# Performance work log

Hardware: AMD Instinct MI355X
Metric: run time of the kernel (lower is better)

The kernel has to match this reference:

```python
import jax, jax.numpy as jnp
import numpy as np

EMBED = 1024
HEADS = 16
HEAD_DIM = EMBED // HEADS
OUT_DIM = 1024


def setup_inputs() -> dict:
    key = jax.random.key(0)
    ks = jax.random.split(key, 8)
    N, L = 2, 2048
    values = jax.random.normal(ks[0], (N, L, EMBED), dtype=jnp.float32)
    keys_t = jax.random.normal(ks[1], (N, L, EMBED), dtype=jnp.float32)
    query = jax.random.normal(ks[2], (N, L, EMBED), dtype=jnp.float32)
    s = 1.0 / np.sqrt(HEAD_DIM)
    Wv = jax.random.normal(ks[3], (HEAD_DIM, HEAD_DIM), dtype=jnp.float32) * s
    Wk = jax.random.normal(ks[4], (HEAD_DIM, HEAD_DIM), dtype=jnp.float32) * s
    Wq = jax.random.normal(ks[5], (HEAD_DIM, HEAD_DIM), dtype=jnp.float32) * s
    Wout = jax.random.normal(ks[6], (OUT_DIM, EMBED), dtype=jnp.float32) * (1.0 / np.sqrt(EMBED))
    bout = jax.random.normal(ks[7], (OUT_DIM,), dtype=jnp.float32) * 0.01
    return {"values": values, "keys": keys_t, "query": query,
            "Wv": Wv, "Wk": Wk, "Wq": Wq, "Wout": Wout, "bout": bout}


def reference(values, keys, query, Wv, Wk, Wq, Wout, bout):
    N, Lq, _ = query.shape
    Lk = keys.shape[1]
    # split into heads: (N, L, H, D)
    v = values.reshape(N, Lk, HEADS, HEAD_DIM)
    k = keys.reshape(N, Lk, HEADS, HEAD_DIM)
    q = query.reshape(N, Lq, HEADS, HEAD_DIM)
    # per-head shared linear projections (torch Linear: x @ W.T, no bias)
    v = jnp.einsum('nlhd,ed->nlhe', v, Wv)
    k = jnp.einsum('nlhd,ed->nlhe', k, Wk)
    q = jnp.einsum('nqhd,ed->nqhe', q, Wq)
    # scores (N, H, Q, K); NOTE: scale is 1/sqrt(embed_size), per original code
    scores = jnp.einsum('nqhd,nkhd->nhqk', q, k) / jnp.sqrt(jnp.float32(EMBED))
    attn = jax.nn.softmax(scores, axis=-1)
    out = jnp.einsum('nhqk,nkhd->nqhd', attn, v).reshape(N, Lq, EMBED)
    # fc_out: x @ Wout.T + bout
    return out @ Wout.T + bout
```

## Files before the change

### kernel.cpp

```cpp
#include <hip/hip_runtime.h>
#include <cstdint>

typedef __attribute__((ext_vector_type(8))) short short8;
typedef __attribute__((ext_vector_type(4))) float floatx4;
typedef __attribute__((ext_vector_type(16))) float floatx16;
typedef __attribute__((ext_vector_type(4))) _Float16 half4;
typedef __attribute__((ext_vector_type(8))) _Float16 half8;

#define DEV __device__ __forceinline__

constexpr int NB = 2, Lseq = 2048, NH = 16, HD = 64, EMB = 1024;
constexpr float QSCALE = 0.03125f * 1.4426950408889634f;

DEV uint32_t pack2(float lo, float hi) {
  uint32_t a = __builtin_bit_cast(uint32_t, lo) + 0x8000u;
  uint32_t b = __builtin_bit_cast(uint32_t, hi) + 0x8000u;
  return __builtin_amdgcn_perm(b, a, 0x07060302);
}

DEV uint32_t packh2(float lo, float hi) {
  return __builtin_bit_cast(uint32_t, __builtin_amdgcn_cvt_pkrtz(lo, hi));
}

DEV void gl_lds16(const void* g, void* l) {
  __builtin_amdgcn_global_load_lds((const __attribute__((address_space(1))) void*)g,
                                   (__attribute__((address_space(3))) void*)l, 16, 0, 0);
}

DEV void pl32(uint32_t& x, uint32_t& y) {
  typedef __attribute__((ext_vector_type(2))) unsigned int uint2v;
  uint2v r = __builtin_amdgcn_permlane32_swap(x, y, false, false);
  x = r[0];
  y = r[1];
}

DEV short8 ld8bf(const float* p, float sc) {
  float4 u = *(const float4*)p;
  float4 v = *(const float4*)(p + 4);
  union { short8 s; uint32_t d[4]; } r;
  r.d[0] = pack2(u.x * sc, u.y * sc);
  r.d[1] = pack2(u.z * sc, u.w * sc);
  r.d[2] = pack2(v.x * sc, v.y * sc);
  r.d[3] = pack2(v.z * sc, v.w * sc);
  return r.s;
}

__global__ __launch_bounds__(256) void prep_kernel(
    const float* __restrict__ values, const float* __restrict__ keysrc,
    const float* __restrict__ query, const float* __restrict__ Wv,
    const float* __restrict__ Wk, const float* __restrict__ Wq,
    const float* __restrict__ Wout,
    uint16_t* __restrict__ qp, uint16_t* __restrict__ kp,
    uint16_t* __restrict__ vp, uint16_t* __restrict__ wbf) {
  const int t = threadIdx.x, w = t >> 6, lane = t & 63;
  const int quad = lane >> 4, l16 = lane & 15;
  const int wid = blockIdx.x * 4 + w;
  const int mat = wid >> 10, sub = wid & 1023;

  if (mat == 3) {
#pragma unroll
    for (int i = 0; i < 4; ++i) {
      int idx = sub * 256 + i * 64 + lane;
      float4 v = ((const float4*)Wout)[idx];
      uint2 p;
      p.x = pack2(v.x, v.y);
      p.y = pack2(v.z, v.w);
      ((uint2*)wbf)[idx] = p;
    }
    return;
  }

  floatx4 c[4][4];
#pragma unroll
  for (int i = 0; i < 4; ++i)
#pragma unroll
    for (int j = 0; j < 4; ++j) c[i][j] = floatx4{0.f, 0.f, 0.f, 0.f};

  if (mat < 2) {
    const float* src = mat ? keysrc : query;
    const float* W   = mat ? Wk : Wq;
    const float asc  = mat ? 1.f : QSCALE;
    uint16_t* dst    = mat ? kp : qp;
    const int R0 = sub * 64;
    short8 a[4][2], b[4][2];
#pragma unroll
    for (int dc = 0; dc < 2; ++dc) {
#pragma unroll
      for (int f = 0; f < 4; ++f) {
        a[f][dc] = ld8bf(W + (size_t)(f * 16 + l16) * 64 + dc * 32 + quad * 8, asc);
        b[f][dc] = ld8bf(src + (size_t)(R0 + f * 16 + l16) * 64 + dc * 32 + quad * 8, 1.f);
      }
    }
#pragma unroll
    for (int dc = 0; dc < 2; ++dc)
#pragma unroll
      for (int mf = 0; mf < 4; ++mf)
#pragma unroll
        for (int nf = 0; nf < 4; ++nf)
          c[mf][nf] = __builtin_amdgcn_mfma_f32_16x16x32_bf16(a[mf][dc], b[nf][dc], c[mf][nf], 0, 0, 0);
#pragma unroll
    for (int nf = 0; nf < 4; ++nf) {
      int r = R0 + nf * 16 + l16;
      int h = r & 15, l = (r >> 4) & 2047, n = r >> 15;
      uint16_t* drow = dst + ((size_t)(n * 16 + h) * 2048 + l) * 64;
#pragma unroll
      for (int mf = 0; mf < 4; ++mf) {
        uint2 pk;
        pk.x = pack2(c[mf][nf][0], c[mf][nf][1]);
        pk.y = pack2(c[mf][nf][2], c[mf][nf][3]);
        *(uint2*)(drow + mf * 16 + quad * 4) = pk;
      }
    }
  } else {
    const int nh = sub >> 5, L0 = (sub & 31) * 64;
    const int n = nh >> 4, h = nh & 15;
    short8 a[4][2], b[4][2];
#pragma unroll
    for (int dc = 0; dc < 2; ++dc) {
#pragma unroll
      for (int f = 0; f < 4; ++f) {
        a[f][dc] = ld8bf(values + (size_t)(n * 2048 + L0 + f * 16 + l16) * 1024 + h * 64 + dc * 32 + quad * 8, 1.f);
        b[f][dc] = ld8bf(Wv + (size_t)(f * 16 + l16) * 64 + dc * 32 + quad * 8, 1.f);
      }
    }
#pragma unroll
    for (int dc = 0; dc < 2; ++dc)
#pragma unroll
      for (int mf = 0; mf < 4; ++mf)
#pragma unroll
        for (int nf = 0; nf < 4; ++nf)
          c[mf][nf] = __builtin_amdgcn_mfma_f32_16x16x32_bf16(a[mf][dc], b[nf][dc], c[mf][nf], 0, 0, 0);
#pragma unroll
    for (int nf = 0; nf < 4; ++nf) {
      int d = nf * 16 + l16;
      uint16_t* drow = vp + ((size_t)nh * 64 + d) * 2048 + L0;
#pragma unroll
      for (int mf = 0; mf < 4; ++mf) {
        uint2 pk;
        pk.x = packh2(c[mf][nf][0], c[mf][nf][1]);
        pk.y = packh2(c[mf][nf][2], c[mf][nf][3]);
        *(uint2*)(drow + mf * 16 + quad * 4) = pk;
      }
    }
  }
}

__global__ __launch_bounds__(128, 2) void flash_kernel(const uint16_t* __restrict__ qp,
                                                       const uint16_t* __restrict__ kp,
                                                       const uint16_t* __restrict__ vp,
                                                       uint16_t* __restrict__ xg) {
  constexpr int kbn = 32;
  __shared__ uint16_t Kt[2][64 * 64];
  __shared__ uint16_t Vt[2][64 * 64];
  const int t = threadIdx.x;
  const int w = t >> 6, lane = t & 63, hi = lane >> 5, l32 = lane & 31;
  const int nh = blockIdx.x, qt = blockIdx.y;
  const int q0w = qt * 64 + w * 32;
  const uint16_t* Qb = qp + (size_t)nh * Lseq * HD;
  const uint16_t* Kb = kp + (size_t)nh * Lseq * HD;
  const uint16_t* Vb = vp + (size_t)nh * HD * Lseq;
  const int srow = lane >> 3, sc8 = (lane & 7) ^ (lane >> 3);

  short8 bq[4];
#pragma unroll
  for (int dc = 0; dc < 4; ++dc)
    bq[dc] = *(const short8*)(Qb + (size_t)(q0w + l32) * 64 + dc * 16 + hi * 8);

  floatx16 o[2], lfr;
#pragma unroll
  for (int r = 0; r < 16; ++r) { o[0][r] = 0.f; o[1][r] = 0.f; lfr[r] = 0.f; }
  const _Float16 one = (_Float16)1.0f;
  const half8 vones = {one, one, one, one, one, one, one, one};

  auto stage = [&](int tile, int buf) {
#pragma unroll
    for (int i = 0; i < 4; ++i) {
      int r0 = w * 32 + i * 8;
      int sc = sc8 ^ i;
      gl_lds16(Kb + (size_t)tile * 4096 + (r0 + srow) * 64 + sc * 8, &Kt[buf][r0 * 64]);
      gl_lds16(Vb + (size_t)(r0 + srow) * Lseq + tile * 64 + sc * 8, &Vt[buf][r0 * 64]);
    }
  };

  stage(0, 0);

  for (int kb = 0; kb < kbn; ++kb) {
    __syncthreads();
    const int cur = kb & 1;
    if (kb + 1 < kbn) stage(kb + 1, cur ^ 1);

#pragma unroll
    for (int kt = 0; kt < 2; ++kt) {
      floatx16 s;
#pragma unroll
      for (int r = 0; r < 16; ++r) s[r] = 0.f;
      const int krow = kt * 32 + l32;
      const int ksw = (krow & 7) ^ ((krow >> 3) & 3);
#pragma unroll
      for (int dc = 0; dc < 4; ++dc) {
        short8 ak = *(const short8*)(&Kt[cur][krow * 64 + (((dc << 1) | hi) ^ ksw) * 8]);
        s = __builtin_amdgcn_mfma_f32_32x32x16_bf16(ak, bq[dc], s, 0, 0, 0);
      }
      uint32_t a0 = packh2(__builtin_amdgcn_exp2f(s[0]), __builtin_amdgcn_exp2f(s[1]));
      uint32_t a1 = packh2(__builtin_amdgcn_exp2f(s[2]), __builtin_amdgcn_exp2f(s[3]));
      uint32_t b0 = packh2(__builtin_amdgcn_exp2f(s[4]), __builtin_amdgcn_exp2f(s[5]));
      uint32_t b1 = packh2(__builtin_amdgcn_exp2f(s[6]), __builtin_amdgcn_exp2f(s[7]));
      uint32_t c0 = packh2(__builtin_amdgcn_exp2f(s[8]), __builtin_amdgcn_exp2f(s[9]));
      uint32_t c1 = packh2(__builtin_amdgcn_exp2f(s[10]), __builtin_amdgcn_exp2f(s[11]));
      uint32_t d0 = packh2(__builtin_amdgcn_exp2f(s[12]), __builtin_amdgcn_exp2f(s[13]));
      uint32_t d1 = packh2(__builtin_amdgcn_exp2f(s[14]), __builtin_amdgcn_exp2f(s[15]));
      pl32(a0, b0); pl32(a1, b1); pl32(c0, d0); pl32(c1, d1);
      union { half8 h; uint32_t u[4]; } f0, f1;
      f0.u[0] = a0; f0.u[1] = a1; f0.u[2] = b0; f0.u[3] = b1;
      f1.u[0] = c0; f1.u[1] = c1; f1.u[2] = d0; f1.u[3] = d1;

      lfr = __builtin_amdgcn_mfma_f32_32x32x16_f16(vones, f0.h, lfr, 0, 0, 0);
      lfr = __builtin_amdgcn_mfma_f32_32x32x16_f16(vones, f1.h, lfr, 0, 0, 0);

#pragma unroll
      for (int dt = 0; dt < 2; ++dt) {
        const int vrow = dt * 32 + l32;
        const int vsw = (vrow & 7) ^ ((vrow >> 3) & 3);
        half8 av0 = *(const half8*)(&Vt[cur][vrow * 64 + ((kt * 4 + hi) ^ vsw) * 8]);
        o[dt] = __builtin_amdgcn_mfma_f32_32x32x16_f16(av0, f0.h, o[dt], 0, 0, 0);
        half8 av1 = *(const half8*)(&Vt[cur][vrow * 64 + ((kt * 4 + 2 + hi) ^ vsw) * 8]);
        o[dt] = __builtin_amdgcn_mfma_f32_32x32x16_f16(av1, f1.h, o[dt], 0, 0, 0);
      }
    }
  }

  const int nn = nh >> 4, h = nh & 15;
  const float inv = __builtin_amdgcn_rcpf(lfr[0]);
  uint16_t* xr = xg + ((size_t)(nn * 2048 + q0w + l32)) * 1024 + h * 64;
#pragma unroll
  for (int dt = 0; dt < 2; ++dt)
#pragma unroll
    for (int rg = 0; rg < 4; ++rg) {
      int dd = dt * 32 + rg * 8 + 4 * hi;
      uint2 pk;
      pk.x = pack2(o[dt][rg * 4] * inv, o[dt][rg * 4 + 1] * inv);
      pk.y = pack2(o[dt][rg * 4 + 2] * inv, o[dt][rg * 4 + 3] * inv);
      *(uint2*)(xr + dd) = pk;
    }
}

__global__ __launch_bounds__(256, 2) void out_gemm(const uint16_t* __restrict__ Xg,
                                                   const uint16_t* __restrict__ Wb,
                                                   const float* __restrict__ bias,
                                                   float* __restrict__ out) {
  __shared__ uint16_t Xt[3][64 * 64];
  __shared__ uint16_t Wt[3][128 * 64];
  const int t = threadIdx.x, w = t >> 6, lane = t & 63, quad = lane >> 4, l16 = lane & 15;
  const int m0 = blockIdx.x * 64, o0 = blockIdx.y * 128;
  const int srow = lane >> 3, sc8 = (lane & 7) ^ (lane >> 3);

  floatx4 acc[8];
#pragma unroll
  for (int j = 0; j < 8; ++j) acc[j] = floatx4{0.f, 0.f, 0.f, 0.f};

  auto stage = [&](int buf, int kt) {
#pragma unroll
    for (int i = 0; i < 2; ++i) {
      int r0 = w * 16 + i * 8;
      gl_lds16(Xg + (size_t)(m0 + r0 + srow) * 1024 + kt * 64 + sc8 * 8, &Xt[buf][r0 * 64]);
    }
#pragma unroll
    for (int i = 0; i < 4; ++i) {
      int r0 = w * 32 + i * 8;
      gl_lds16(Wb + (size_t)(o0 + r0 + srow) * 1024 + kt * 64 + sc8 * 8, &Wt[buf][r0 * 64]);
    }
  };

  stage(0, 0);
  stage(1, 1);

  int cur = 0;
  for (int kt = 0; kt < 16; ++kt) {
    if (kt + 1 < 16) asm volatile("s_waitcnt vmcnt(6)" ::: "memory");
    else             asm volatile("s_waitcnt vmcnt(0)" ::: "memory");
    __builtin_amdgcn_s_barrier();
    if (kt + 2 < 16) {
      int tgt = cur + 2; if (tgt >= 3) tgt -= 3;
      stage(tgt, kt + 2);
    }
#pragma unroll
    for (int kc = 0; kc < 2; ++kc) {
      int ra = w * 16 + l16;
      short8 a = *(const short8*)(&Xt[cur][ra * 64 + ((kc * 4 + quad) ^ (ra & 7)) * 8]);
#pragma unroll
      for (int nf = 0; nf < 8; ++nf) {
        int rb = nf * 16 + l16;
        short8 b = *(const short8*)(&Wt[cur][rb * 64 + ((kc * 4 + quad) ^ (rb & 7)) * 8]);
        acc[nf] = __builtin_amdgcn_mfma_f32_16x16x32_bf16(a, b, acc[nf], 0, 0, 0);
      }
    }
    asm volatile("s_waitcnt lgkmcnt(0)" ::: "memory");
    cur = (cur + 1 == 3) ? 0 : cur + 1;
  }

#pragma unroll
  for (int nf = 0; nf < 8; ++nf) {
    float bv = bias[o0 + nf * 16 + l16];
#pragma unroll
    for (int r = 0; r < 4; ++r)
      out[(size_t)(m0 + w * 16 + quad * 4 + r) * 1024 + o0 + nf * 16 + l16] = acc[nf][r] + bv;
  }
}

extern "C" void kernel_launch(void* const* d_in, const int* in_sizes, int n_in,
                              void* d_out, int out_size, void* d_ws, size_t ws_size,
                              hipStream_t stream) {
  const float* values = (const float*)d_in[0];
  const float* keys   = (const float*)d_in[1];
  const float* query  = (const float*)d_in[2];
  const float* Wv     = (const float*)d_in[3];
  const float* Wk     = (const float*)d_in[4];
  const float* Wq     = (const float*)d_in[5];
  const float* Wout   = (const float*)d_in[6];
  const float* bout   = (const float*)d_in[7];
  float* out = (float*)d_out;
  (void)ws_size;

  uint16_t* ws  = (uint16_t*)d_ws;
  uint16_t* qp  = ws;
  uint16_t* kp  = ws + (size_t)4194304;
  uint16_t* vp  = ws + (size_t)8388608;
  uint16_t* wbf = ws + (size_t)12582912;
  uint16_t* xp  = ws + (size_t)13631488;

  prep_kernel<<<dim3(1024), dim3(256), 0, stream>>>(values, keys, query, Wv, Wk, Wq, Wout,
                                                    qp, kp, vp, wbf);
  flash_kernel<<<dim3(32, 32), dim3(128), 0, stream>>>(qp, kp, vp, xp);
  out_gemm<<<dim3(64, 8), dim3(256), 0, stream>>>(xp, wbf, bout, out);
}
```

Measured before the change: 185.1 us.

## Split attention over key halves and merge partials in output GEMM prologue

The flash kernel now splits the key range into two halves along a third grid dimension and uses 4-wave blocks covering 128 queries. Each half writes unnormalized fp16 partial outputs and row sums to the workspace. The output GEMM loads both partials, adds them, normalizes, and packs to bf16 in LDS before the MFMA loop, so the separate normalized activation buffer is no longer written. This aims for better occupancy and more K/V reuse per block, at the cost of extra partial-output traffic, more work in the GEMM prologue, and fp16 accumulation of unnormalized sums.

```diff
diff --git a/kernel.cpp b/kernel.cpp
--- a/kernel.cpp
+++ b/kernel.cpp
@@ -4,7 +4,6 @@
 typedef __attribute__((ext_vector_type(8))) short short8;
 typedef __attribute__((ext_vector_type(4))) float floatx4;
 typedef __attribute__((ext_vector_type(16))) float floatx16;
-typedef __attribute__((ext_vector_type(4))) _Float16 half4;
 typedef __attribute__((ext_vector_type(8))) _Float16 half8;
 
 #define DEV __device__ __forceinline__
@@ -145,20 +144,22 @@
   }
 }
 
-__global__ __launch_bounds__(128, 2) void flash_kernel(const uint16_t* __restrict__ qp,
+__global__ __launch_bounds__(256, 4) void flash_kernel(const uint16_t* __restrict__ qp,
                                                        const uint16_t* __restrict__ kp,
                                                        const uint16_t* __restrict__ vp,
-                                                       uint16_t* __restrict__ xg) {
-  constexpr int kbn = 32;
+                                                       uint32_t* __restrict__ opart,
+                                                       float* __restrict__ psum) {
+  constexpr int kbn = 16;
   __shared__ uint16_t Kt[2][64 * 64];
   __shared__ uint16_t Vt[2][64 * 64];
   const int t = threadIdx.x;
   const int w = t >> 6, lane = t & 63, hi = lane >> 5, l32 = lane & 31;
-  const int nh = blockIdx.x, qt = blockIdx.y;
-  const int q0w = qt * 64 + w * 32;
+  const int nh = blockIdx.x, qt = blockIdx.y, kh = blockIdx.z;
+  const int q0w = qt * 128 + w * 32;
   const uint16_t* Qb = qp + (size_t)nh * Lseq * HD;
-  const uint16_t* Kb = kp + (size_t)nh * Lseq * HD;
+  const uint16_t* Kb = kp + (size_t)nh * Lseq * HD + (size_t)kh * 1024 * 64;
   const uint16_t* Vb = vp + (size_t)nh * HD * Lseq;
+  const int vcol0 = kh * 1024;
   const int srow = lane >> 3, sc8 = (lane & 7) ^ (lane >> 3);
 
   short8 bq[4];
@@ -174,11 +175,11 @@
 
   auto stage = [&](int tile, int buf) {
 #pragma unroll
-    for (int i = 0; i < 4; ++i) {
-      int r0 = w * 32 + i * 8;
-      int sc = sc8 ^ i;
+    for (int i = 0; i < 2; ++i) {
+      int r0 = w * 16 + i * 8;
+      int sc = sc8 ^ ((w * 2 + i) & 3);
       gl_lds16(Kb + (size_t)tile * 4096 + (r0 + srow) * 64 + sc * 8, &Kt[buf][r0 * 64]);
-      gl_lds16(Vb + (size_t)(r0 + srow) * Lseq + tile * 64 + sc * 8, &Vt[buf][r0 * 64]);
+      gl_lds16(Vb + (size_t)(r0 + srow) * Lseq + vcol0 + tile * 64 + sc * 8, &Vt[buf][r0 * 64]);
     }
   };
 
@@ -229,41 +230,75 @@
     }
   }
 
-  const int nn = nh >> 4, h = nh & 15;
-  const float inv = __builtin_amdgcn_rcpf(lfr[0]);
-  uint16_t* xr = xg + ((size_t)(nn * 2048 + q0w + l32)) * 1024 + h * 64;
+  uint32_t* ob = opart + ((size_t)(((nh * 16 + qt) * 2 + kh) * 4 + w)) * 1024 + lane;
 #pragma unroll
   for (int dt = 0; dt < 2; ++dt)
 #pragma unroll
-    for (int rg = 0; rg < 4; ++rg) {
-      int dd = dt * 32 + rg * 8 + 4 * hi;
-      uint2 pk;
-      pk.x = pack2(o[dt][rg * 4] * inv, o[dt][rg * 4 + 1] * inv);
-      pk.y = pack2(o[dt][rg * 4 + 2] * inv, o[dt][rg * 4 + 3] * inv);
-      *(uint2*)(xr + dd) = pk;
-    }
-}
-
-__global__ __launch_bounds__(256, 2) void out_gemm(const uint16_t* __restrict__ Xg,
+    for (int j = 0; j < 8; ++j)
+      ob[(dt * 8 + j) * 64] = packh2(o[dt][2 * j], o[dt][2 * j + 1]);
+  if (hi == 0)
+    psum[((size_t)((nh * 16 + qt) * 2 + kh)) * 128 + w * 32 + l32] = lfr[0];
+}
+
+__global__ __launch_bounds__(256, 2) void out_gemm(const uint32_t* __restrict__ opart,
+                                                   const float* __restrict__ psum,
                                                    const uint16_t* __restrict__ Wb,
                                                    const float* __restrict__ bias,
                                                    float* __restrict__ out) {
-  __shared__ uint16_t Xt[3][64 * 64];
-  __shared__ uint16_t Wt[3][128 * 64];
+  __shared__ uint16_t Xt[64 * 64];
+  __shared__ uint16_t Wt[2][128 * 64];
   const int t = threadIdx.x, w = t >> 6, lane = t & 63, quad = lane >> 4, l16 = lane & 15;
-  const int m0 = blockIdx.x * 64, o0 = blockIdx.y * 128;
+  const int mblk = blockIdx.x, obk = blockIdx.y;
+  const int nrow = mblk >> 5, qt_src = (mblk & 31) >> 1;
+  const int m0 = mblk * 64, o0 = obk * 128;
+  const int w_src = (mblk & 1) * 2 + (w >> 1);
+  const int kh_l = lane >> 5;
+  const int hi_l = (lane >> 4) & 1;
+  const int l32s = (w & 1) * 16 + (lane & 15);
+  const int src_lane = kh_l * 0 + hi_l * 32 + l32s;
   const int srow = lane >> 3, sc8 = (lane & 7) ^ (lane >> 3);
 
   floatx4 acc[8];
 #pragma unroll
   for (int j = 0; j < 8; ++j) acc[j] = floatx4{0.f, 0.f, 0.f, 0.f};
 
-  auto stage = [&](int buf, int kt) {
-#pragma unroll
-    for (int i = 0; i < 2; ++i) {
-      int r0 = w * 16 + i * 8;
-      gl_lds16(Xg + (size_t)(m0 + r0 + srow) * 1024 + kt * 64 + sc8 * 8, &Xt[buf][r0 * 64]);
-    }
+  uint32_t va[16];
+  float lp;
+
+  auto issue_loads = [&](int h) {
+    int nh2 = nrow * 16 + h;
+    size_t tb = (size_t)((nh2 * 16 + qt_src) * 2 + kh_l);
+    const uint32_t* pa = opart + (tb * 4 + w_src) * 1024 + src_lane;
+#pragma unroll
+    for (int k = 0; k < 16; ++k) va[k] = pa[k * 64];
+    lp = psum[tb * 128 + w_src * 32 + l32s];
+  };
+
+  auto pack_write = [&]() {
+    uint32_t lx = __builtin_bit_cast(uint32_t, lp), ly = lx;
+    pl32(lx, ly);
+    float lpart = __builtin_bit_cast(float, (lane < 32) ? ly : lx);
+    float inv = __builtin_amdgcn_rcpf(lp + lpart);
+    const int ra = w * 16 + (lane & 15);
+    const int rsw = ra & 7;
+#pragma unroll
+    for (int k = 0; k < 16; ++k) {
+      const int dt = k >> 3, j = k & 7;
+      uint32_t own = va[k], x = own, y = own;
+      pl32(x, y);
+      uint32_t part = (lane < 32) ? y : x;
+      union { uint32_t u; _Float16 h[2]; } um, up;
+      um.u = own; up.u = part;
+      float v0 = ((float)um.h[0] + (float)up.h[0]) * inv;
+      float v1 = ((float)um.h[1] + (float)up.h[1]) * inv;
+      const int d0t = (j & 1) * 2 + (j >> 1) * 8;
+      const int d = dt * 32 + d0t + 4 * hi_l;
+      if (lane < 32)
+        *(uint32_t*)(&Xt[ra * 64 + ((d >> 3) ^ rsw) * 8 + (d & 7)]) = pack2(v0, v1);
+    }
+  };
+
+  auto dma_w = [&](int buf, int kt) {
 #pragma unroll
     for (int i = 0; i < 4; ++i) {
       int r0 = w * 32 + i * 8;
@@ -271,22 +306,21 @@
     }
   };
 
-  stage(0, 0);
-  stage(1, 1);
-
-  int cur = 0;
+  issue_loads(0);
+  pack_write();
+  dma_w(0, 0);
+
   for (int kt = 0; kt < 16; ++kt) {
-    if (kt + 1 < 16) asm volatile("s_waitcnt vmcnt(6)" ::: "memory");
-    else             asm volatile("s_waitcnt vmcnt(0)" ::: "memory");
-    __builtin_amdgcn_s_barrier();
-    if (kt + 2 < 16) {
-      int tgt = cur + 2; if (tgt >= 3) tgt -= 3;
-      stage(tgt, kt + 2);
+    const int cur = kt & 1;
+    __syncthreads();
+    if (kt + 1 < 16) {
+      issue_loads(kt + 1);
+      dma_w(cur ^ 1, kt + 1);
     }
 #pragma unroll
     for (int kc = 0; kc < 2; ++kc) {
       int ra = w * 16 + l16;
-      short8 a = *(const short8*)(&Xt[cur][ra * 64 + ((kc * 4 + quad) ^ (ra & 7)) * 8]);
+      short8 a = *(const short8*)(&Xt[ra * 64 + ((kc * 4 + quad) ^ (ra & 7)) * 8]);
 #pragma unroll
       for (int nf = 0; nf < 8; ++nf) {
         int rb = nf * 16 + l16;
@@ -294,8 +328,7 @@
         acc[nf] = __builtin_amdgcn_mfma_f32_16x16x32_bf16(a, b, acc[nf], 0, 0, 0);
       }
     }
-    asm volatile("s_waitcnt lgkmcnt(0)" ::: "memory");
-    cur = (cur + 1 == 3) ? 0 : cur + 1;
+    if (kt + 1 < 16) pack_write();
   }
 
 #pragma unroll
@@ -326,10 +359,11 @@
   uint16_t* kp  = ws + (size_t)4194304;
   uint16_t* vp  = ws + (size_t)8388608;
   uint16_t* wbf = ws + (size_t)12582912;
-  uint16_t* xp  = ws + (size_t)13631488;
+  uint32_t* opart = (uint32_t*)(ws + (size_t)13631488);
+  float* psum = (float*)(ws + (size_t)13631488 + 8388608);
 
   prep_kernel<<<dim3(1024), dim3(256), 0, stream>>>(values, keys, query, Wv, Wk, Wq, Wout,
                                                     qp, kp, vp, wbf);
-  flash_kernel<<<dim3(32, 32), dim3(128), 0, stream>>>(qp, kp, vp, xp);
-  out_gemm<<<dim3(64, 8), dim3(256), 0, stream>>>(xp, wbf, bout, out);
-}
+  flash_kernel<<<dim3(32, 16, 2), dim3(256), 0, stream>>>(qp, kp, vp, opart, psum);
+  out_gemm<<<dim3(64, 8), dim3(256), 0, stream>>>(opart, psum, wbf, bout, out);
+}
```

Measured after the change: 185.5 us. About the same (+0.2%).

## Split flash attention over key halves with 4-wave blocks and combine kernel

Applied to the files above, without the earlier changes.

The flash kernel now uses 256-thread blocks covering 128 queries, and splits the key sequence into two halves along a third grid dimension. Each half writes unnormalized fp16 partial outputs and row sums to workspace. A new combine kernel adds the two halves, normalizes, and writes the bf16 attention output through swizzled LDS with coalesced stores. The aim is better K/V tile reuse across more waves and more parallel blocks. The cost is an extra kernel launch and partial-result traffic. Summing without a max is safe only because the original also skips max subtraction.

```diff
diff --git a/kernel.cpp b/kernel.cpp
--- a/kernel.cpp
+++ b/kernel.cpp
@@ -4,7 +4,6 @@
 typedef __attribute__((ext_vector_type(8))) short short8;
 typedef __attribute__((ext_vector_type(4))) float floatx4;
 typedef __attribute__((ext_vector_type(16))) float floatx16;
-typedef __attribute__((ext_vector_type(4))) _Float16 half4;
 typedef __attribute__((ext_vector_type(8))) _Float16 half8;
 
 #define DEV __device__ __forceinline__
@@ -145,20 +144,22 @@
   }
 }
 
-__global__ __launch_bounds__(128, 2) void flash_kernel(const uint16_t* __restrict__ qp,
+__global__ __launch_bounds__(256, 4) void flash_kernel(const uint16_t* __restrict__ qp,
                                                        const uint16_t* __restrict__ kp,
                                                        const uint16_t* __restrict__ vp,
-                                                       uint16_t* __restrict__ xg) {
-  constexpr int kbn = 32;
+                                                       uint32_t* __restrict__ opart,
+                                                       float* __restrict__ psum) {
+  constexpr int kbn = 16;
   __shared__ uint16_t Kt[2][64 * 64];
   __shared__ uint16_t Vt[2][64 * 64];
   const int t = threadIdx.x;
   const int w = t >> 6, lane = t & 63, hi = lane >> 5, l32 = lane & 31;
-  const int nh = blockIdx.x, qt = blockIdx.y;
-  const int q0w = qt * 64 + w * 32;
+  const int nh = blockIdx.x, qt = blockIdx.y, kh = blockIdx.z;
+  const int q0w = qt * 128 + w * 32;
   const uint16_t* Qb = qp + (size_t)nh * Lseq * HD;
-  const uint16_t* Kb = kp + (size_t)nh * Lseq * HD;
+  const uint16_t* Kb = kp + (size_t)nh * Lseq * HD + (size_t)kh * 1024 * 64;
   const uint16_t* Vb = vp + (size_t)nh * HD * Lseq;
+  const int vcol0 = kh * 1024;
   const int srow = lane >> 3, sc8 = (lane & 7) ^ (lane >> 3);
 
   short8 bq[4];
@@ -174,11 +175,11 @@
 
   auto stage = [&](int tile, int buf) {
 #pragma unroll
-    for (int i = 0; i < 4; ++i) {
-      int r0 = w * 32 + i * 8;
-      int sc = sc8 ^ i;
+    for (int i = 0; i < 2; ++i) {
+      int r0 = w * 16 + i * 8;
+      int sc = sc8 ^ ((w * 2 + i) & 3);
       gl_lds16(Kb + (size_t)tile * 4096 + (r0 + srow) * 64 + sc * 8, &Kt[buf][r0 * 64]);
-      gl_lds16(Vb + (size_t)(r0 + srow) * Lseq + tile * 64 + sc * 8, &Vt[buf][r0 * 64]);
+      gl_lds16(Vb + (size_t)(r0 + srow) * Lseq + vcol0 + tile * 64 + sc * 8, &Vt[buf][r0 * 64]);
     }
   };
 
@@ -229,19 +230,54 @@
     }
   }
 
+  uint32_t* ob = opart + ((size_t)(((nh * 16 + qt) * 2 + kh) * 4 + w)) * 1024 + lane;
+#pragma unroll
+  for (int dt = 0; dt < 2; ++dt)
+#pragma unroll
+    for (int j = 0; j < 8; ++j)
+      ob[(dt * 8 + j) * 64] = packh2(o[dt][2 * j], o[dt][2 * j + 1]);
+  if (hi == 0)
+    psum[((size_t)((nh * 16 + qt) * 2 + kh)) * 128 + w * 32 + l32] = lfr[0];
+}
+
+__global__ __launch_bounds__(256) void combine_kernel(const uint32_t* __restrict__ opart,
+                                                      const float* __restrict__ psum,
+                                                      uint16_t* __restrict__ xg) {
+  __shared__ uint32_t Xs[128 * 32];
+  const int t = threadIdx.x, w = t >> 6, lane = t & 63;
+  const int hi = lane >> 5, l32 = lane & 31;
+  const int nh = blockIdx.x, qt = blockIdx.y;
+  const size_t tb0 = (size_t)((nh * 16 + qt) * 2);
+  const uint32_t* pa0 = opart + (tb0 * 4 + w) * 1024 + lane;
+  const uint32_t* pa1 = opart + ((tb0 + 1) * 4 + w) * 1024 + lane;
+  const float l0 = psum[tb0 * 128 + w * 32 + l32];
+  const float l1 = psum[(tb0 + 1) * 128 + w * 32 + l32];
+  const float inv = __builtin_amdgcn_rcpf(l0 + l1);
+  const int ql = w * 32 + l32;
+
+#pragma unroll
+  for (int k = 0; k < 16; ++k) {
+    const int dt = k >> 3, j = k & 7;
+    union { uint32_t u; _Float16 h[2]; } u0, u1;
+    u0.u = pa0[k * 64];
+    u1.u = pa1[k * 64];
+    float v0 = ((float)u0.h[0] + (float)u1.h[0]) * inv;
+    float v1 = ((float)u0.h[1] + (float)u1.h[1]) * inv;
+    const int d = dt * 32 + (j >> 1) * 8 + (j & 1) * 2 + 4 * hi;
+    Xs[ql * 32 + ((d >> 1) ^ ((ql & 7) << 2))] = pack2(v0, v1);
+  }
+  __syncthreads();
+
   const int nn = nh >> 4, h = nh & 15;
-  const float inv = __builtin_amdgcn_rcpf(lfr[0]);
-  uint16_t* xr = xg + ((size_t)(nn * 2048 + q0w + l32)) * 1024 + h * 64;
-#pragma unroll
-  for (int dt = 0; dt < 2; ++dt)
-#pragma unroll
-    for (int rg = 0; rg < 4; ++rg) {
-      int dd = dt * 32 + rg * 8 + 4 * hi;
-      uint2 pk;
-      pk.x = pack2(o[dt][rg * 4] * inv, o[dt][rg * 4 + 1] * inv);
-      pk.y = pack2(o[dt][rg * 4 + 2] * inv, o[dt][rg * 4 + 3] * inv);
-      *(uint2*)(xr + dd) = pk;
-    }
+#pragma unroll
+  for (int pass = 0; pass < 2; ++pass) {
+    int row = pass * 64 + (t >> 2), l4 = t & 3;
+    uint4 v = *(const uint4*)(&Xs[row * 32 + ((l4 * 8) ^ ((row & 7) << 2))]);
+    uint4 v2 = *(const uint4*)(&Xs[row * 32 + (((l4 * 8 + 4)) ^ ((row & 7) << 2))]);
+    uint16_t* xr = xg + ((size_t)(nn * 2048 + qt * 128 + row)) * 1024 + h * 64 + l4 * 16;
+    *(uint4*)xr = v;
+    *(uint4*)(xr + 8) = v2;
+  }
 }
 
 __global__ __launch_bounds__(256, 2) void out_gemm(const uint16_t* __restrict__ Xg,
@@ -326,10 +362,13 @@
   uint16_t* kp  = ws + (size_t)4194304;
   uint16_t* vp  = ws + (size_t)8388608;
   uint16_t* wbf = ws + (size_t)12582912;
-  uint16_t* xp  = ws + (size_t)13631488;
+  uint32_t* opart = (uint32_t*)(ws + (size_t)13631488);
+  float* psum = (float*)(ws + (size_t)22020096);
+  uint16_t* xp  = ws + (size_t)22282240;
 
   prep_kernel<<<dim3(1024), dim3(256), 0, stream>>>(values, keys, query, Wv, Wk, Wq, Wout,
                                                     qp, kp, vp, wbf);
-  flash_kernel<<<dim3(32, 32), dim3(128), 0, stream>>>(qp, kp, vp, xp);
+  flash_kernel<<<dim3(32, 16, 2), dim3(256), 0, stream>>>(qp, kp, vp, opart, psum);
+  combine_kernel<<<dim3(32, 16), dim3(256), 0, stream>>>(opart, psum, xp);
   out_gemm<<<dim3(64, 8), dim3(256), 0, stream>>>(xp, wbf, bout, out);
 }
```

Measured after the change: 178.6 us. 1.04x faster.
